# Kernel tuning notes

Measured on AMD Instinct MI355X. Metric: run time of the kernel, lower is better.

## Reference

```python
import jax, jax.numpy as jnp
import numpy as np

B, N, C = 16, 1024, 256
NH, DH = 8, 32          # dense attention heads
NHD, P = 8, 4           # deformable heads / sampling points
Hs = Ws = 32            # value spatial grid (N == Hs*Ws)
HID = 1024              # mlp hidden = 4*C


def setup_inputs() -> dict:
    key = jax.random.key(0)
    ks = jax.random.split(key, 16)
    rn = lambda i, shape, s=1.0: jax.random.normal(ks[i], shape, jnp.float32) * s
    return {
        "x": rn(0, (B, N, C)),
        "ref": jax.random.uniform(ks[1], (B, N, 2), jnp.float32),
        "value": rn(2, (B, N, C)),
        "ln1_w": jnp.ones((C,), jnp.float32), "ln1_b": jnp.zeros((C,), jnp.float32),
        "ln2_w": jnp.ones((C,), jnp.float32), "ln2_b": jnp.zeros((C,), jnp.float32),
        "ln3_w": jnp.ones((C,), jnp.float32), "ln3_b": jnp.zeros((C,), jnp.float32),
        "qkv_w": rn(3, (3 * C, C), 0.05),
        "proj_w": rn(4, (C, C), 0.05), "proj_b": jnp.zeros((C,), jnp.float32),
        "off_w": rn(5, (NHD * P * 2, C), 0.01), "off_b": rn(6, (NHD * P * 2,), 0.5),
        "aw_w": rn(7, (NHD * P, C), 0.01), "aw_b": jnp.zeros((NHD * P,), jnp.float32),
        "vproj_w": rn(8, (C, C), 0.05), "vproj_b": jnp.zeros((C,), jnp.float32),
        "oproj_w": rn(9, (C, C), 0.05), "oproj_b": jnp.zeros((C,), jnp.float32),
        "fc1_w": rn(10, (HID, C), 0.05), "fc1_b": jnp.zeros((HID,), jnp.float32),
        "fc2_w": rn(11, (C, HID), 0.05), "fc2_b": jnp.zeros((C,), jnp.float32),
    }


def _ln(x, w, b):
    m = x.mean(-1, keepdims=True)
    v = ((x - m) ** 2).mean(-1, keepdims=True)
    return (x - m) * jax.lax.rsqrt(v + 1e-5) * w + b


def _attn(x, qkv_w, proj_w, proj_b):
    qkv = (x @ qkv_w.T).reshape(B, N, 3, NH, DH)
    q, k, v = qkv[:, :, 0], qkv[:, :, 1], qkv[:, :, 2]
    a = jnp.einsum('bqhd,bkhd->bhqk', q, k) * (DH ** -0.5)
    a = jax.nn.softmax(a, axis=-1)
    o = jnp.einsum('bhqk,bkhd->bqhd', a, v).reshape(B, N, C)
    return o @ proj_w.T + proj_b


def _deform(q, ref, value, off_w, off_b, aw_w, aw_b, vproj_w, vproj_b, oproj_w, oproj_b):
    # single-level MS deformable attention (Deformable-DETR style)
    v = (value @ vproj_w.T + vproj_b).reshape(B, Hs * Ws, NHD, DH)
    off = (q @ off_w.T + off_b).reshape(B, N, NHD, P, 2)
    aw = jax.nn.softmax((q @ aw_w.T + aw_b).reshape(B, N, NHD, P), axis=-1)
    norm = jnp.array([Ws, Hs], jnp.float32)
    loc = ref[:, :, None, None, :] + off / norm  # [B,N,NHD,P,2] normalized coords
    gx = loc[..., 0] * Ws - 0.5
    gy = loc[..., 1] * Hs - 0.5
    x0 = jnp.floor(gx); y0 = jnp.floor(gy)
    lx = gx - x0; ly = gy - y0
    x0i = x0.astype(jnp.int32); y0i = y0.astype(jnp.int32)
    b_idx = jnp.arange(B)[:, None, None, None]
    h_idx = jnp.arange(NHD)[None, None, :, None]

    def gather(xi, yi):
        valid = ((xi >= 0) & (xi < Ws) & (yi >= 0) & (yi < Hs)).astype(jnp.float32)
        idx = jnp.clip(yi, 0, Hs - 1) * Ws + jnp.clip(xi, 0, Ws - 1)
        return v[b_idx, idx, h_idx] * valid[..., None]  # [B,N,NHD,P,DH]

    s = (gather(x0i, y0i) * ((1 - lx) * (1 - ly))[..., None]
         + gather(x0i + 1, y0i) * (lx * (1 - ly))[..., None]
         + gather(x0i, y0i + 1) * ((1 - lx) * ly)[..., None]
         + gather(x0i + 1, y0i + 1) * (lx * ly)[..., None])
    out = (s * aw[..., None]).sum(axis=3).reshape(B, N, C)
    return out @ oproj_w.T + oproj_b


def reference(x, ref, value, ln1_w, ln1_b, ln2_w, ln2_b, ln3_w, ln3_b,
              qkv_w, proj_w, proj_b, off_w, off_b, aw_w, aw_b,
              vproj_w, vproj_b, oproj_w, oproj_b, fc1_w, fc1_b, fc2_w, fc2_b):
    x = x + _attn(_ln(x, ln1_w, ln1_b), qkv_w, proj_w, proj_b)
    x = x + _deform(_ln(x, ln2_w, ln2_b), ref, value,
                    off_w, off_b, aw_w, aw_b, vproj_w, vproj_b, oproj_w, oproj_b)
    h = jax.nn.gelu(_ln(x, ln3_w, ln3_b) @ fc1_w.T + fc1_b, approximate=False) @ fc2_w.T + fc2_b
    return x + h
```

## Files before the change

### kernel.cpp

```cpp
#include <hip/hip_runtime.h>
#include <hip/hip_bf16.h>

#define Bq   16
#define Nq   1024
#define Cq   256
#define NHq  8
#define DHq  32
#define HIDq 1024
#define BNq  (Bq * Nq)

typedef float f32x4 __attribute__((ext_vector_type(4)));
typedef short bf16x8 __attribute__((ext_vector_type(8)));
typedef unsigned short ushort_t;

__device__ __forceinline__ unsigned int f2bf(float f) {
    unsigned int u = __builtin_bit_cast(unsigned int, f);
    u = (u + 0x7fffu + ((u >> 16) & 1u)) >> 16;
    return u & 0xffffu;
}
__device__ __forceinline__ unsigned int packbf2(float a, float b) {
    unsigned int ua = __builtin_bit_cast(unsigned int, a) + 0x8000u;
    unsigned int ub = __builtin_bit_cast(unsigned int, b) + 0x8000u;
    return __builtin_amdgcn_perm(ub, ua, 0x07060302);
}
__device__ __forceinline__ float gelu_t(float x) {
    float y = x * (0.7978845608028654f + 0.035677408136300125f * x * x);
    float e = __builtin_amdgcn_exp2f(y * 2.8853900817779268f);
    return x - x / (1.f + e);
}

typedef __attribute__((address_space(1))) const unsigned int* gas_u32;
typedef __attribute__((address_space(3))) unsigned int* las_u32;
__device__ __forceinline__ void gload16(const void* g, void* l) {
    __builtin_amdgcn_global_load_lds((gas_u32)g, (las_u32)l, 16, 0, 0);
}

struct CastSeg { const float* src; ushort_t* dst; int nblk; int n; };
struct CastArgs { CastSeg s[9]; };

__global__ __launch_bounds__(256) void castm(CastArgs a) {
    int bid = blockIdx.x;
    int seg = 0, acc = 0;
    for (seg = 0; seg < 9; seg++) {
        if (bid < acc + a.s[seg].nblk) break;
        acc += a.s[seg].nblk;
    }
    const CastSeg sg = a.s[seg];
    int i = (bid - acc) * 1024 + threadIdx.x * 4;
    if (i < sg.n) {
        float4 v = *(const float4*)(sg.src + i);
        uint2 u;
        u.x = packbf2(v.x, v.y);
        u.y = packbf2(v.z, v.w);
        *(uint2*)(sg.dst + i) = u;
    }
}

__global__ __launch_bounds__(256) void ln_kernel(const float* __restrict__ X,
                                                 const float* __restrict__ w,
                                                 const float* __restrict__ b,
                                                 ushort_t* __restrict__ Y) {
    int wave = threadIdx.x >> 6, lane = threadIdx.x & 63;
    int t = blockIdx.x * 4 + wave;
    float4 v = *(const float4*)(X + (size_t)t * Cq + lane * 4);
    float s = v.x + v.y + v.z + v.w;
#pragma unroll
    for (int d = 1; d < 64; d <<= 1) s += __shfl_xor(s, d);
    float mean = s * (1.f / 256.f);
    float4 dv = {v.x - mean, v.y - mean, v.z - mean, v.w - mean};
    float q = dv.x * dv.x + dv.y * dv.y + dv.z * dv.z + dv.w * dv.w;
#pragma unroll
    for (int d = 1; d < 64; d <<= 1) q += __shfl_xor(q, d);
    float rs = rsqrtf(q * (1.f / 256.f) + 1e-5f);
    float4 wv = *(const float4*)(w + lane * 4);
    float4 bv = *(const float4*)(b + lane * 4);
    uint2 u;
    u.x = packbf2(dv.x * rs * wv.x + bv.x, dv.y * rs * wv.y + bv.y);
    u.y = packbf2(dv.z * rs * wv.z + bv.z, dv.w * rs * wv.w + bv.w);
    *(uint2*)(Y + (size_t)t * Cq + lane * 4) = u;
}

template <int OMODE, bool GELU_, bool RESID, int KT>
__global__ __launch_bounds__(256) void mgemm(const ushort_t* __restrict__ A,
                                             const ushort_t* __restrict__ W,
                                             const float* __restrict__ bias,
                                             const float* __restrict__ R,
                                             void* __restrict__ OutP,
                                             int M, int Nn) {
    __shared__ __align__(16) ushort_t Al[8192];
    __shared__ __align__(16) ushort_t Bl[8192];
    int m0 = blockIdx.x * 128, n0 = blockIdx.y * 128;
    int tid = threadIdx.x;
    int w = tid >> 6, lane = tid & 63;
    int l15 = lane & 15, quad = lane >> 4;
    int wrow = w >> 1, wcol = w & 1;

    f32x4 acc[4][4];
#pragma unroll
    for (int i = 0; i < 4; i++)
#pragma unroll
        for (int j = 0; j < 4; j++) acc[i][j] = (f32x4){0.f, 0.f, 0.f, 0.f};

    const ushort_t* gA0 = A + (size_t)(m0 + lane) * KT + w * 8;
    const ushort_t* gA1 = A + (size_t)(m0 + 64 + lane) * KT + w * 8;
    const ushort_t* gB0 = W + (size_t)(n0 + lane) * KT + w * 8;
    const ushort_t* gB1 = W + (size_t)(n0 + 64 + lane) * KT + w * 8;
    ushort_t* lA0  = &Al[(w * 128) * 8];
    ushort_t* lA1  = &Al[(w * 128 + 64) * 8];
    ushort_t* lA0h = &Al[((w + 4) * 128) * 8];
    ushort_t* lA1h = &Al[((w + 4) * 128 + 64) * 8];
    ushort_t* lB0  = &Bl[(w * 128) * 8];
    ushort_t* lB1  = &Bl[(w * 128 + 64) * 8];
    ushort_t* lB0h = &Bl[((w + 4) * 128) * 8];
    ushort_t* lB1h = &Bl[((w + 4) * 128 + 64) * 8];

#pragma unroll
    for (int k0 = 0; k0 < KT; k0 += 64) {
        gload16(gA0 + k0, lA0);
        gload16(gA1 + k0, lA1);
        gload16(gA0 + k0 + 32, lA0h);
        gload16(gA1 + k0 + 32, lA1h);
        gload16(gB0 + k0, lB0);
        gload16(gB1 + k0, lB1);
        gload16(gB0 + k0 + 32, lB0h);
        gload16(gB1 + k0 + 32, lB1h);
        __syncthreads();

#pragma unroll
        for (int ks = 0; ks < 2; ks++) {
            bf16x8 aF[4], bF[4];
#pragma unroll
            for (int i = 0; i < 4; i++)
                aF[i] = *(const bf16x8*)&Al[((ks * 4 + quad) * 128 + wrow * 64 + i * 16 + l15) * 8];
#pragma unroll
            for (int j = 0; j < 4; j++)
                bF[j] = *(const bf16x8*)&Bl[((ks * 4 + quad) * 128 + wcol * 64 + j * 16 + l15) * 8];
#pragma unroll
            for (int i = 0; i < 4; i++)
#pragma unroll
                for (int j = 0; j < 4; j++)
                    acc[i][j] = __builtin_amdgcn_mfma_f32_16x16x32_bf16(bF[j], aF[i], acc[i][j], 0, 0, 0);
        }
        __syncthreads();
    }

#pragma unroll
    for (int i = 0; i < 4; i++) {
        int mg = m0 + wrow * 64 + i * 16 + l15;
#pragma unroll
        for (int j = 0; j < 4; j++) {
            int ng = n0 + wcol * 64 + j * 16 + quad * 4;
            f32x4 rv = acc[i][j];
            if constexpr (OMODE == 1) {
                int which = ng >> 8;
                int h = (ng >> 5) & 7;
                int d = ng & 31;
                int bb = mg >> 10, nn = mg & 1023;
                ushort_t* qb = (ushort_t*)OutP;
                if (which == 2) {
                    size_t dst = 2 * (size_t)BNq * Cq +
                                 ((size_t)(bb * 8 + h) * 32 + d) * 1024 + nn;
#pragma unroll
                    for (int r = 0; r < 4; r++)
                        qb[dst + (size_t)r * 1024] = (ushort_t)f2bf(rv[r]);
                } else {
                    if (which == 0) {
                        const float sc = 0.17677669529663687f * 1.4426950408889634f;
                        rv[0] *= sc; rv[1] *= sc; rv[2] *= sc; rv[3] *= sc;
                    }
                    size_t dst = (size_t)which * ((size_t)BNq * Cq) +
                                 ((size_t)(bb * 8 + h) * 1024 + nn) * 32 + d;
                    uint2 pk;
                    pk.x = packbf2(rv[0], rv[1]);
                    pk.y = packbf2(rv[2], rv[3]);
                    *(uint2*)(qb + dst) = pk;
                }
            } else if constexpr (OMODE == 3) {
                if (ng >= 96) continue;
                if (ng < 64) {
                    float4 bv = *(const float4*)(bias + ng);
                    rv[0] += bv.x; rv[1] += bv.y; rv[2] += bv.z; rv[3] += bv.w;
                    *(float4*)((float*)OutP + (size_t)mg * 64 + ng) =
                        make_float4(rv[0], rv[1], rv[2], rv[3]);
                } else {
                    float4 bv = *(const float4*)(R + (ng - 64));
                    rv[0] += bv.x; rv[1] += bv.y; rv[2] += bv.z; rv[3] += bv.w;
                    *(float4*)((float*)OutP + (size_t)BNq * 64 + (size_t)mg * 32 + (ng - 64)) =
                        make_float4(rv[0], rv[1], rv[2], rv[3]);
                }
            } else {
                if (bias) {
                    float4 bv = *(const float4*)(bias + ng);
                    rv[0] += bv.x; rv[1] += bv.y; rv[2] += bv.z; rv[3] += bv.w;
                }
                if (GELU_) {
#pragma unroll
                    for (int r = 0; r < 4; r++) rv[r] = gelu_t(rv[r]);
                }
                if constexpr (OMODE == 2) {
                    uint2 pk;
                    pk.x = packbf2(rv[0], rv[1]);
                    pk.y = packbf2(rv[2], rv[3]);
                    *(uint2*)((ushort_t*)OutP + (size_t)mg * Nn + ng) = pk;
                } else {
                    if (RESID) {
                        float4 rr = *(const float4*)(R + (size_t)mg * Nn + ng);
                        rv[0] += rr.x; rv[1] += rr.y; rv[2] += rr.z; rv[3] += rr.w;
                    }
                    *(float4*)((float*)OutP + (size_t)mg * Nn + ng) =
                        make_float4(rv[0], rv[1], rv[2], rv[3]);
                }
            }
        }
    }
}

__global__ __launch_bounds__(256) void attn_mfma(const ushort_t* __restrict__ Qb,
                                                 const ushort_t* __restrict__ Kb,
                                                 const ushort_t* __restrict__ Vtg,
                                                 ushort_t* __restrict__ o) {
    int bh = blockIdx.x;
    int b = bh >> 3, h = bh & 7;
    int q0 = blockIdx.y * 128;
    int tid = threadIdx.x;
    int wave = tid >> 6, lane = tid & 63;
    int l15 = lane & 15, quad = lane >> 4;

    __shared__ __align__(16) ushort_t Ks[64][40];
    __shared__ __align__(16) ushort_t Vs[32][88];
    __shared__ __align__(16) ushort_t Ps[4][32][72];

    const size_t hb = (size_t)bh * 32768;

    bf16x8 qfrag[2];
#pragma unroll
    for (int g = 0; g < 2; g++)
        qfrag[g] = *(const bf16x8*)(Qb + hb + (size_t)(q0 + wave * 32 + g * 16 + l15) * 32 + quad * 8);

    f32x4 oa[2][2];
#pragma unroll
    for (int g = 0; g < 2; g++)
#pragma unroll
        for (int t = 0; t < 2; t++) oa[g][t] = (f32x4){0.f, 0.f, 0.f, 0.f};
    float lsum[2] = {0.f, 0.f};

    int krow = tid >> 2, kch = tid & 3;
    int vrow = tid >> 3, vch = tid & 7;
    const ushort_t* kgp = Kb + hb + (size_t)krow * 32 + kch * 8;
    const ushort_t* vgp = Vtg + hb + (size_t)vrow * 1024 + vch * 8;

    for (int kt = 0; kt < 16; kt++) {
        __syncthreads();
        *(bf16x8*)&Ks[krow][kch * 8] = *(const bf16x8*)(kgp + kt * 64 * 32);
        *(bf16x8*)&Vs[vrow][vch * 8] = *(const bf16x8*)(vgp + kt * 64);
        __syncthreads();

        bf16x8 kf[4];
#pragma unroll
        for (int kg = 0; kg < 4; kg++)
            kf[kg] = *(const bf16x8*)&Ks[kg * 16 + l15][quad * 8];

        const f32x4 z = {0.f, 0.f, 0.f, 0.f};
#pragma unroll
        for (int g = 0; g < 2; g++) {
#pragma unroll
            for (int kg = 0; kg < 4; kg++) {
                f32x4 st = __builtin_amdgcn_mfma_f32_16x16x32_bf16(kf[kg], qfrag[g], z, 0, 0, 0);
                float e0 = __builtin_amdgcn_exp2f(st[0]);
                float e1 = __builtin_amdgcn_exp2f(st[1]);
                float e2 = __builtin_amdgcn_exp2f(st[2]);
                float e3 = __builtin_amdgcn_exp2f(st[3]);
                lsum[g] += (e0 + e1) + (e2 + e3);
                uint2 pk;
                pk.x = packbf2(e0, e1);
                pk.y = packbf2(e2, e3);
                *(uint2*)&Ps[wave][g * 16 + l15][kg * 16 + quad * 4] = pk;
            }
        }
#pragma unroll
        for (int c = 0; c < 2; c++) {
            bf16x8 vb0 = *(const bf16x8*)&Vs[l15][c * 32 + quad * 8];
            bf16x8 vb1 = *(const bf16x8*)&Vs[16 + l15][c * 32 + quad * 8];
#pragma unroll
            for (int g = 0; g < 2; g++) {
                bf16x8 pa = *(const bf16x8*)&Ps[wave][g * 16 + l15][c * 32 + quad * 8];
                oa[g][0] = __builtin_amdgcn_mfma_f32_16x16x32_bf16(pa, vb0, oa[g][0], 0, 0, 0);
                oa[g][1] = __builtin_amdgcn_mfma_f32_16x16x32_bf16(pa, vb1, oa[g][1], 0, 0, 0);
            }
        }
    }

#pragma unroll
    for (int g = 0; g < 2; g++) {
        float rs = lsum[g];
        rs += __shfl_xor(rs, 16);
        rs += __shfl_xor(rs, 32);
        lsum[g] = rs;
    }
#pragma unroll
    for (int g = 0; g < 2; g++) {
#pragma unroll
        for (int r = 0; r < 4; r++) {
            float inv = 1.f / __shfl(lsum[g], quad * 4 + r);
            int q = q0 + wave * 32 + g * 16 + quad * 4 + r;
            ushort_t* orow = o + ((size_t)(b * 1024 + q)) * 256 + h * 32;
            orow[l15] = (ushort_t)f2bf(oa[g][0][r] * inv);
            orow[l15 + 16] = (ushort_t)f2bf(oa[g][1][r] * inv);
        }
    }
}

__global__ __launch_bounds__(256) void deform_kernel(const float* __restrict__ ref,
                                                     const float* __restrict__ off,
                                                     const float* __restrict__ awl,
                                                     const float* __restrict__ v,
                                                     ushort_t* __restrict__ out) {
    int t = blockIdx.x;
    int b = t >> 10;
    int tid = threadIdx.x;
    int h = tid >> 5, d = tid & 31;

    float rx = ref[(size_t)t * 2 + 0];
    float ry = ref[(size_t)t * 2 + 1];
    const float* offr = off + (size_t)t * 64 + h * 8;
    const float* awr = awl + (size_t)t * 32 + h * 4;

    float L0 = awr[0], L1 = awr[1], L2 = awr[2], L3 = awr[3];
    float mm = fmaxf(fmaxf(L0, L1), fmaxf(L2, L3));
    float e0 = __expf(L0 - mm), e1 = __expf(L1 - mm), e2 = __expf(L2 - mm), e3 = __expf(L3 - mm);
    float inv = 1.f / (e0 + e1 + e2 + e3);
    float aw[4] = {e0 * inv, e1 * inv, e2 * inv, e3 * inv};

    const float* vb = v + (size_t)b * Nq * Cq + h * 32 + d;

    float s = 0.f;
#pragma unroll
    for (int p = 0; p < 4; p++) {
        float gx = rx * 32.f + offr[p * 2 + 0] - 0.5f;
        float gy = ry * 32.f + offr[p * 2 + 1] - 0.5f;
        float x0f = floorf(gx), y0f = floorf(gy);
        float lx = gx - x0f, ly = gy - y0f;
        int x0 = (int)x0f, y0 = (int)y0f;
        auto g = [&](int xi, int yi) -> float {
            if (xi < 0 || xi > 31 || yi < 0 || yi > 31) return 0.f;
            return vb[(size_t)(yi * 32 + xi) * Cq];
        };
        float sp = g(x0, y0) * (1.f - lx) * (1.f - ly)
                 + g(x0 + 1, y0) * lx * (1.f - ly)
                 + g(x0, y0 + 1) * (1.f - lx) * ly
                 + g(x0 + 1, y0 + 1) * lx * ly;
        s += aw[p] * sp;
    }
    out[(size_t)t * Cq + h * 32 + d] = (ushort_t)f2bf(s);
}

extern "C" void kernel_launch(void* const* d_in, const int* in_sizes, int n_in,
                              void* d_out, int out_size, void* d_ws, size_t ws_size,
                              hipStream_t stream) {
    const size_t S = (size_t)BNq * Cq;
    float* ws = (float*)d_ws;
    float* X = ws;
    ushort_t* Ybf = (ushort_t*)(ws + S);
    ushort_t* Wbf = (ushort_t*)(ws + S + S / 2);

    ushort_t* Wqkv   = Wbf;
    ushort_t* Wproj  = Wbf + 196608;
    ushort_t* Woff   = Wbf + 262144;
    ushort_t* Waw    = Wbf + 278528;
    ushort_t* Wvproj = Wbf + 286720;
    ushort_t* Woproj = Wbf + 352256;
    ushort_t* Wfc1   = Wbf + 417792;
    ushort_t* Wfc2   = Wbf + 679936;

    ushort_t* QKVbf = (ushort_t*)(ws + 2 * S);
    ushort_t* O1bf  = (ushort_t*)(ws + 2 * S + 3 * S / 2);
    float* Vb   = ws + 2 * S + S / 2;
    float* OffB = ws + 2 * S + 3 * S / 2;
    float* AwB  = OffB + (size_t)BNq * 64;
    ushort_t* Sbbf = (ushort_t*)(AwB + (size_t)BNq * 32);
    ushort_t* Hbbf = (ushort_t*)(ws + 2 * S);
    ushort_t* Valbf = (ushort_t*)(ws + 9 * S / 2);

    auto fp = [&](int i) { return (const float*)d_in[i]; };
    const float* x_in = fp(0);

    CastArgs ca;
    ca.s[0] = {fp(9),  Wqkv,   192, 196608};
    ca.s[1] = {fp(10), Wproj,  64,  65536};
    ca.s[2] = {fp(12), Woff,   16,  16384};
    ca.s[3] = {fp(14), Waw,    8,   8192};
    ca.s[4] = {fp(16), Wvproj, 64,  65536};
    ca.s[5] = {fp(18), Woproj, 64,  65536};
    ca.s[6] = {fp(20), Wfc1,   256, 262144};
    ca.s[7] = {fp(22), Wfc2,   256, 262144};
    ca.s[8] = {fp(2),  Valbf,  4096, (int)S};
    castm<<<5016, 256, 0, stream>>>(ca);

    ln_kernel<<<BNq / 4, 256, 0, stream>>>(x_in, fp(3), fp(4), Ybf);
    mgemm<1, false, false, 256><<<dim3(128, 6), 256, 0, stream>>>(
        Ybf, Wqkv, nullptr, nullptr, QKVbf, BNq, 768);
    attn_mfma<<<dim3(128, 8), 256, 0, stream>>>(
        QKVbf, QKVbf + S, QKVbf + 2 * S, O1bf);
    mgemm<0, false, true, 256><<<dim3(128, 2), 256, 0, stream>>>(
        O1bf, Wproj, fp(11), x_in, X, BNq, 256);

    ln_kernel<<<BNq / 4, 256, 0, stream>>>(X, fp(5), fp(6), Ybf);
    mgemm<0, false, false, 256><<<dim3(128, 2), 256, 0, stream>>>(
        Valbf, Wvproj, fp(17), nullptr, Vb, BNq, 256);
    mgemm<3, false, false, 256><<<dim3(128, 1), 256, 0, stream>>>(
        Ybf, Woff, fp(13), fp(15), OffB, BNq, 96);
    deform_kernel<<<BNq, 256, 0, stream>>>(fp(1), OffB, AwB, Vb, Sbbf);
    mgemm<0, false, true, 256><<<dim3(128, 2), 256, 0, stream>>>(
        Sbbf, Woproj, fp(19), X, X, BNq, 256);

    ln_kernel<<<BNq / 4, 256, 0, stream>>>(X, fp(7), fp(8), Ybf);
    mgemm<2, true, false, 256><<<dim3(128, 8), 256, 0, stream>>>(
        Ybf, Wfc1, fp(21), nullptr, Hbbf, BNq, 1024);
    mgemm<0, false, true, 1024><<<dim3(128, 2), 256, 0, stream>>>(
        Hbbf, Wfc2, fp(23), X, d_out, BNq, 256);
}
```

Baseline: 344.8 us.

## Double-buffer GEMM and attention tiles, compute softmax sums via MFMA

The GEMM main loop now uses a 32-wide k-step with two LDS buffers, so the next tile's global-to-LDS load is issued while the current tile is multiplied, and one barrier per step is removed. Attention keeps K/V in double-buffered LDS with register prefetch, so each iteration needs one barrier instead of two. Row sums now come from an extra MFMA against a vector of ones, which removes the scalar adds and cross-lane shuffles, and the bf16 pack uses the hardware cvt_pk instruction. It also adds setprio around the PV MFMAs and raises the attention launch-bounds occupancy hint. The risks are extra MFMA work, the row sum now being taken over bf16-rounded probabilities, and a possible LDS hazard, because the GEMM issues the next async load without a barrier after the compute.

```diff
diff --git a/kernel.cpp b/kernel.cpp
--- a/kernel.cpp
+++ b/kernel.cpp
@@ -22,6 +22,11 @@
     unsigned int ua = __builtin_bit_cast(unsigned int, a) + 0x8000u;
     unsigned int ub = __builtin_bit_cast(unsigned int, b) + 0x8000u;
     return __builtin_amdgcn_perm(ub, ua, 0x07060302);
+}
+__device__ __forceinline__ unsigned int cvtpk_bf16(float lo, float hi) {
+    unsigned int r;
+    asm("v_cvt_pk_bf16_f32 %0, %1, %2" : "=v"(r) : "v"(lo), "v"(hi));
+    return r;
 }
 __device__ __forceinline__ float gelu_t(float x) {
     float y = x * (0.7978845608028654f + 0.035677408136300125f * x * x);
@@ -105,42 +110,41 @@
     const ushort_t* gA1 = A + (size_t)(m0 + 64 + lane) * KT + w * 8;
     const ushort_t* gB0 = W + (size_t)(n0 + lane) * KT + w * 8;
     const ushort_t* gB1 = W + (size_t)(n0 + 64 + lane) * KT + w * 8;
-    ushort_t* lA0  = &Al[(w * 128) * 8];
-    ushort_t* lA1  = &Al[(w * 128 + 64) * 8];
-    ushort_t* lA0h = &Al[((w + 4) * 128) * 8];
-    ushort_t* lA1h = &Al[((w + 4) * 128 + 64) * 8];
-    ushort_t* lB0  = &Bl[(w * 128) * 8];
-    ushort_t* lB1  = &Bl[(w * 128 + 64) * 8];
-    ushort_t* lB0h = &Bl[((w + 4) * 128) * 8];
-    ushort_t* lB1h = &Bl[((w + 4) * 128 + 64) * 8];
-
-#pragma unroll
-    for (int k0 = 0; k0 < KT; k0 += 64) {
-        gload16(gA0 + k0, lA0);
-        gload16(gA1 + k0, lA1);
-        gload16(gA0 + k0 + 32, lA0h);
-        gload16(gA1 + k0 + 32, lA1h);
-        gload16(gB0 + k0, lB0);
-        gload16(gB1 + k0, lB1);
-        gload16(gB0 + k0 + 32, lB0h);
-        gload16(gB1 + k0 + 32, lB1h);
-        __syncthreads();
-
-#pragma unroll
-        for (int ks = 0; ks < 2; ks++) {
-            bf16x8 aF[4], bF[4];
-#pragma unroll
-            for (int i = 0; i < 4; i++)
-                aF[i] = *(const bf16x8*)&Al[((ks * 4 + quad) * 128 + wrow * 64 + i * 16 + l15) * 8];
+    ushort_t* lA0 = &Al[(w * 128) * 8];
+    ushort_t* lA1 = &Al[(w * 128 + 64) * 8];
+    ushort_t* lB0 = &Bl[(w * 128) * 8];
+    ushort_t* lB1 = &Bl[(w * 128 + 64) * 8];
+    constexpr int BUFO = 4096;
+
+    gload16(gA0, lA0);
+    gload16(gA1, lA1);
+    gload16(gB0, lB0);
+    gload16(gB1, lB1);
+    __syncthreads();
+
+    constexpr int NT = KT / 32;
+#pragma unroll
+    for (int t = 0; t < NT; t++) {
+        const int cur = (t & 1) * BUFO;
+        const int nxt = ((t + 1) & 1) * BUFO;
+        if (t + 1 < NT) {
+            gload16(gA0 + (t + 1) * 32, lA0 + nxt);
+            gload16(gA1 + (t + 1) * 32, lA1 + nxt);
+            gload16(gB0 + (t + 1) * 32, lB0 + nxt);
+            gload16(gB1 + (t + 1) * 32, lB1 + nxt);
+        }
+        bf16x8 aF[4], bF[4];
+#pragma unroll
+        for (int i = 0; i < 4; i++)
+            aF[i] = *(const bf16x8*)&Al[cur + (quad * 128 + wrow * 64 + i * 16 + l15) * 8];
+#pragma unroll
+        for (int j = 0; j < 4; j++)
+            bF[j] = *(const bf16x8*)&Bl[cur + (quad * 128 + wcol * 64 + j * 16 + l15) * 8];
+#pragma unroll
+        for (int i = 0; i < 4; i++)
 #pragma unroll
             for (int j = 0; j < 4; j++)
-                bF[j] = *(const bf16x8*)&Bl[((ks * 4 + quad) * 128 + wcol * 64 + j * 16 + l15) * 8];
-#pragma unroll
-            for (int i = 0; i < 4; i++)
-#pragma unroll
-                for (int j = 0; j < 4; j++)
-                    acc[i][j] = __builtin_amdgcn_mfma_f32_16x16x32_bf16(bF[j], aF[i], acc[i][j], 0, 0, 0);
-        }
+                acc[i][j] = __builtin_amdgcn_mfma_f32_16x16x32_bf16(bF[j], aF[i], acc[i][j], 0, 0, 0);
         __syncthreads();
     }
 
@@ -215,10 +219,10 @@
     }
 }
 
-__global__ __launch_bounds__(256) void attn_mfma(const ushort_t* __restrict__ Qb,
-                                                 const ushort_t* __restrict__ Kb,
-                                                 const ushort_t* __restrict__ Vtg,
-                                                 ushort_t* __restrict__ o) {
+__global__ __launch_bounds__(256, 4) void attn_mfma(const ushort_t* __restrict__ Qb,
+                                                    const ushort_t* __restrict__ Kb,
+                                                    const ushort_t* __restrict__ Vtg,
+                                                    ushort_t* __restrict__ o) {
     int bh = blockIdx.x;
     int b = bh >> 3, h = bh & 7;
     int q0 = blockIdx.y * 128;
@@ -226,8 +230,8 @@
     int wave = tid >> 6, lane = tid & 63;
     int l15 = lane & 15, quad = lane >> 4;
 
-    __shared__ __align__(16) ushort_t Ks[64][40];
-    __shared__ __align__(16) ushort_t Vs[32][88];
+    __shared__ __align__(16) ushort_t Ks[2][64][40];
+    __shared__ __align__(16) ushort_t Vs[2][32][88];
     __shared__ __align__(16) ushort_t Ps[4][32][72];
 
     const size_t hb = (size_t)bh * 32768;
@@ -242,23 +246,37 @@
     for (int g = 0; g < 2; g++)
 #pragma unroll
         for (int t = 0; t < 2; t++) oa[g][t] = (f32x4){0.f, 0.f, 0.f, 0.f};
-    float lsum[2] = {0.f, 0.f};
+    f32x4 ls[2];
+    ls[0] = (f32x4){0.f, 0.f, 0.f, 0.f};
+    ls[1] = (f32x4){0.f, 0.f, 0.f, 0.f};
+
+    bf16x8 ones;
+#pragma unroll
+    for (int i = 0; i < 8; i++) ones[i] = (short)0x3F80;
 
     int krow = tid >> 2, kch = tid & 3;
     int vrow = tid >> 3, vch = tid & 7;
     const ushort_t* kgp = Kb + hb + (size_t)krow * 32 + kch * 8;
     const ushort_t* vgp = Vtg + hb + (size_t)vrow * 1024 + vch * 8;
 
+    bf16x8 kreg = *(const bf16x8*)kgp;
+    bf16x8 vreg = *(const bf16x8*)vgp;
+
+#pragma unroll 2
     for (int kt = 0; kt < 16; kt++) {
+        const int cur = kt & 1;
+        *(bf16x8*)&Ks[cur][krow][kch * 8] = kreg;
+        *(bf16x8*)&Vs[cur][vrow][vch * 8] = vreg;
         __syncthreads();
-        *(bf16x8*)&Ks[krow][kch * 8] = *(const bf16x8*)(kgp + kt * 64 * 32);
-        *(bf16x8*)&Vs[vrow][vch * 8] = *(const bf16x8*)(vgp + kt * 64);
-        __syncthreads();
+        if (kt < 15) {
+            kreg = *(const bf16x8*)(kgp + (kt + 1) * 2048);
+            vreg = *(const bf16x8*)(vgp + (kt + 1) * 64);
+        }
 
         bf16x8 kf[4];
 #pragma unroll
         for (int kg = 0; kg < 4; kg++)
-            kf[kg] = *(const bf16x8*)&Ks[kg * 16 + l15][quad * 8];
+            kf[kg] = *(const bf16x8*)&Ks[cur][kg * 16 + l15][quad * 8];
 
         const f32x4 z = {0.f, 0.f, 0.f, 0.f};
 #pragma unroll
@@ -270,38 +288,34 @@
                 float e1 = __builtin_amdgcn_exp2f(st[1]);
                 float e2 = __builtin_amdgcn_exp2f(st[2]);
                 float e3 = __builtin_amdgcn_exp2f(st[3]);
-                lsum[g] += (e0 + e1) + (e2 + e3);
                 uint2 pk;
-                pk.x = packbf2(e0, e1);
-                pk.y = packbf2(e2, e3);
+                pk.x = cvtpk_bf16(e0, e1);
+                pk.y = cvtpk_bf16(e2, e3);
                 *(uint2*)&Ps[wave][g * 16 + l15][kg * 16 + quad * 4] = pk;
             }
         }
+
+        __builtin_amdgcn_s_setprio(1);
 #pragma unroll
         for (int c = 0; c < 2; c++) {
-            bf16x8 vb0 = *(const bf16x8*)&Vs[l15][c * 32 + quad * 8];
-            bf16x8 vb1 = *(const bf16x8*)&Vs[16 + l15][c * 32 + quad * 8];
+            bf16x8 vb0 = *(const bf16x8*)&Vs[cur][l15][c * 32 + quad * 8];
+            bf16x8 vb1 = *(const bf16x8*)&Vs[cur][16 + l15][c * 32 + quad * 8];
 #pragma unroll
             for (int g = 0; g < 2; g++) {
                 bf16x8 pa = *(const bf16x8*)&Ps[wave][g * 16 + l15][c * 32 + quad * 8];
                 oa[g][0] = __builtin_amdgcn_mfma_f32_16x16x32_bf16(pa, vb0, oa[g][0], 0, 0, 0);
                 oa[g][1] = __builtin_amdgcn_mfma_f32_16x16x32_bf16(pa, vb1, oa[g][1], 0, 0, 0);
+                ls[g]    = __builtin_amdgcn_mfma_f32_16x16x32_bf16(pa, ones, ls[g], 0, 0, 0);
             }
         }
+        __builtin_amdgcn_s_setprio(0);
     }
 
 #pragma unroll
     for (int g = 0; g < 2; g++) {
-        float rs = lsum[g];
-        rs += __shfl_xor(rs, 16);
-        rs += __shfl_xor(rs, 32);
-        lsum[g] = rs;
-    }
-#pragma unroll
-    for (int g = 0; g < 2; g++) {
 #pragma unroll
         for (int r = 0; r < 4; r++) {
-            float inv = 1.f / __shfl(lsum[g], quad * 4 + r);
+            float inv = 1.f / ls[g][r];
             int q = q0 + wave * 32 + g * 16 + quad * 4 + r;
             ushort_t* orow = o + ((size_t)(b * 1024 + q)) * 256 + h * 32;
             orow[l15] = (ushort_t)f2bf(oa[g][0][r] * inv);
```

After: 337.7 us. 1.02x faster.
